# Performance work log

Hardware: AMD Instinct MI355X
Metric: run time of the kernel (lower is better)

The kernel has to match this reference:

```python
import jax, jax.numpy as jnp
import numpy as np

TWO_PI = 2.0 * np.pi
EPS = 1e-6

# mixture packed layout along last axis (7): [weight, px, py, cxx, cxy, cyx, cyy]

def unpack(m):
    w = m[..., 0]
    p = m[..., 1:3]
    C = m[..., 3:7].reshape(m.shape[:-1] + (2, 2))
    return w, p, C

def pack(w, p, C):
    return jnp.concatenate([w[..., None], p, C.reshape(C.shape[:-2] + (4,))], axis=-1)

def det2(C):
    return C[..., 0, 0] * C[..., 1, 1] - C[..., 0, 1] * C[..., 1, 0]

def inv2(C):
    d = det2(C)[..., None, None]
    adj = jnp.stack([
        jnp.stack([C[..., 1, 1], -C[..., 0, 1]], axis=-1),
        jnp.stack([-C[..., 1, 0], C[..., 0, 0]], axis=-1)], axis=-2)
    return adj / d

def component_integrals(w, C):
    # integral of an amplitude-parameterized 2D gaussian: w * 2*pi * sqrt(det C)
    return w * TWO_PI * jnp.sqrt(jnp.maximum(det2(C), EPS))

def gm_convolve(data, kernel):
    # data [B,Li,Nd,7], kernel [Lo,Li,Nk,7] -> [B,Lo,Li*Nd*Nk,7]
    wd, pd, Cd = unpack(data)
    wk, pk, Ck = unpack(kernel)
    dd = det2(Cd)[:, None, :, :, None]              # [B,1,Li,Nd,1]
    dk = det2(Ck)[None, :, :, None, :]              # [1,Lo,Li,1,Nk]
    Cs = Cd[:, None, :, :, None, :, :] + Ck[None, :, :, None, :, :, :]  # [B,Lo,Li,Nd,Nk,2,2]
    ps = pd[:, None, :, :, None, :] + pk[None, :, :, None, :, :]        # [B,Lo,Li,Nd,Nk,2]
    # amplitude of convolved gaussian so that integrals multiply
    ws = (wd[:, None, :, :, None] * wk[None, :, :, None, :]
          * TWO_PI * jnp.sqrt(dd * dk / jnp.maximum(det2(Cs), EPS)))
    m = pack(ws, ps, Cs)
    B, Lo = m.shape[0], m.shape[1]
    return m.reshape(B, Lo, -1, 7)

def eval_at_centers(w, p, C):
    # value of the whole mixture at each component center; [.., N]
    Ci = inv2(C)                                        # [..,N,2,2]
    diff = p[..., :, None, :] - p[..., None, :, :]      # [..,K,N,2]
    md = jnp.einsum('...kni,...nij,...knj->...kn', diff, Ci, diff)
    return jnp.einsum('...n,...kn->...k', w, jnp.exp(-0.5 * md))

def relu_fit(m, bias, n_out):
    # fitting-based ReLU: rescale each component so the mixture matches
    # relu(m(x)+b) at the centers, then keep the n_out largest components
    w, p, C = unpack(m)
    v = eval_at_centers(w, p, C) + bias[None, :, None]  # [B,L,N]
    scale = jax.nn.relu(v) / (jnp.abs(v) + EPS)
    w2 = w * scale
    _, idx = jax.lax.top_k(jnp.abs(w2), n_out)          # [B,L,n_out]
    w_s = jnp.take_along_axis(w2, idx, axis=-1)
    p_s = jnp.take_along_axis(p, jnp.broadcast_to(idx[..., None], idx.shape + (2,)), axis=-2)
    Cf = C.reshape(C.shape[:-2] + (4,))
    C_s = jnp.take_along_axis(Cf, jnp.broadcast_to(idx[..., None], idx.shape + (4,)), axis=-2)
    return pack(w_s, p_s, C_s.reshape(C_s.shape[:-1] + (2, 2)))

def batchnorm(m, per_gaussian):
    w, p, C = unpack(m)
    tot = jnp.sum(jnp.abs(component_integrals(w, C)), axis=-1, keepdims=True)  # [B,L,1]
    if not per_gaussian:
        tot = jnp.mean(tot, axis=0, keepdims=True)      # batch statistic per channel
    return pack(w / (tot + EPS), p, C)

def integrate(m):
    w, _, C = unpack(m)
    return jnp.sum(component_integrals(w, C), axis=-1)  # [B,L]

def forward(in_x, kernel1, kernel2, kernel3, bias1, bias2, bias3):
    x = batchnorm(in_x, per_gaussian=True)   # bn0
    x = gm_convolve(x, kernel1)              # [B,5,320,7]
    x = relu_fit(x, bias1, 25)
    x = batchnorm(x, per_gaussian=False)
    x = gm_convolve(x, kernel2)              # [B,6,625,7]
    x = relu_fit(x, bias2, 12)
    x = batchnorm(x, per_gaussian=False)
    x = gm_convolve(x, kernel3)              # [B,10,360,7]
    x = relu_fit(x, bias3, 5)
    x = batchnorm(x, per_gaussian=False)
    out = jax.nn.log_softmax(integrate(x), axis=1)
    return out.reshape(-1, 10)

def _make_kernel(key, lo, li, nk, weight_sd, position_range, covariance_range):
    kw, kp = jax.random.split(key)
    w = jax.random.normal(kw, (lo, li, nk)) * weight_sd
    p = jax.random.uniform(kp, (lo, li, nk, 2), minval=-position_range, maxval=position_range)
    C = jnp.broadcast_to(covariance_range * jnp.eye(2), (lo, li, nk, 2, 2))
    return pack(w, p, C).astype(jnp.float32)

def setup_inputs() -> dict:
    key = jax.random.key(0)
    k = jax.random.split(key, 8)
    B, NIN, NK = 32, 64, 5
    w = jax.random.uniform(k[0], (B, 1, NIN), minval=0.05, maxval=1.0)
    p = jax.random.uniform(k[1], (B, 1, NIN, 2), minval=-14.0, maxval=14.0)
    cdiag = jax.random.uniform(k[2], (B, 1, NIN, 2), minval=0.5, maxval=2.0)
    C = jnp.zeros((B, 1, NIN, 2, 2)).at[..., 0, 0].set(cdiag[..., 0]).at[..., 1, 1].set(cdiag[..., 1])
    in_x = pack(w, p, C).astype(jnp.float32)
    return {
        'in_x': in_x,
        'kernel1': _make_kernel(k[3], 5, 1, NK, 0.4, 2.0, 0.5),
        'kernel2': _make_kernel(k[4], 6, 5, NK, 0.04, 4.0, 2.0),
        'kernel3': _make_kernel(k[5], 10, 6, NK, 0.025, 8.0, 4.0),
        'bias1': jnp.zeros((5,), jnp.float32),
        'bias2': jnp.zeros((6,), jnp.float32),
        'bias3': jnp.zeros((10,), jnp.float32),
    }

def reference(in_x, kernel1, kernel2, kernel3, bias1, bias2, bias3):
    return forward(in_x, kernel1, kernel2, kernel3, bias1, bias2, bias3)
```

## Files before the change

### kernel.cpp

```cpp
#include <hip/hip_runtime.h>

#define TWO_PI_F 6.283185307179586f
#define EPS_F 1e-6f
#define LOG2E_F 1.4426950408889634f
#define BATCH 32

__device__ __forceinline__ float sane(float x) {
    return ((__float_as_uint(x) & 0x7f800000u) == 0x7f800000u) ? 0.f : x;
}

template<int LO, int LI, int ND, int NK, int NCOMP, int KOUT,
         int KP, int TPG, int G, bool FIRST>
__global__ __launch_bounds__(TPG*G) void layer_kernel(
    const float* __restrict__ in_x,
    const float* __restrict__ prev_sel,
    const float* __restrict__ prev_tot,
    const float* __restrict__ kern,
    const float* __restrict__ bias,
    float* __restrict__ out_sel,
    float* __restrict__ out_tot)
{
    constexpr int KUSE   = NCOMP / KP;
    static_assert(KUSE * KP == NCOMP, "exact k tiling required");
    constexpr int CHUNK  = (NCOMP + G - 1) / G;
    constexpr int NCOMP4 = (NCOMP + 3) & ~3;
    constexpr int NQ     = NCOMP4 / 4;
    constexpr int CQ     = (NQ + G - 1) / G;

    const int b   = blockIdx.x / LO;
    const int lo  = blockIdx.x % LO;
    const int tid = threadIdx.x;
    const int g   = tid / TPG;
    const int kt  = tid % TPG;
    const bool active = (kt < KUSE);

    struct StageT {
        float4 d_c[LI*ND];
        float4 k_c[LI*NK];
        float  d_w[LI*ND], d_px[LI*ND], d_py[LI*ND];
        float  k_w[LI*NK], k_px[LI*NK], k_py[LI*NK];
    };
    constexpr size_t ACCB = (size_t)(G > 1 ? (G-1)*TPG*KP : 1) * sizeof(float);
    constexpr size_t UB   = sizeof(StageT) > ACCB ? sizeof(StageT) : ACCB;
    __shared__ __align__(16) unsigned char u_smem[UB];
    StageT& st    = *reinterpret_cast<StageT*>(u_smem);
    float* accbuf = reinterpret_cast<float*>(u_smem);

    __shared__ float2 cPos[NCOMP];
    __shared__ float4 nP[NCOMP];
    __shared__ float4 nQ[NCOMP];
    __shared__ float4 cC[NCOMP];
    __shared__ float  w2s[NCOMP];
    __shared__ __align__(16) float a2s[NCOMP4];
    __shared__ float  scr[64];
    __shared__ float  selint[32];
    __shared__ float  dscale[LI];

    if constexpr (FIRST) {
        if (tid < ND) {
            const float* s = in_x + (size_t)(b*ND + tid)*7;
            const float w  = sane(s[0]);
            const float c0 = sane(s[3]), c1 = sane(s[4]), c2 = sane(s[5]), c3 = sane(s[6]);
            st.d_w[tid] = w; st.d_px[tid] = sane(s[1]); st.d_py[tid] = sane(s[2]);
            st.d_c[tid] = make_float4(c0, c1, c2, c3);
            const float det = c0*c3 - c1*c2;
            scr[tid] = sane(fabsf(w) * TWO_PI_F * sqrtf(fmaxf(det, EPS_F)));
        }
        __syncthreads();
        if (tid == 0) {
            float s = 0.f;
            for (int i = 0; i < ND; ++i) s += scr[i];
            dscale[0] = 1.f / (s + EPS_F);
        }
        __syncthreads();
        if (tid < ND) st.d_w[tid] = sane(st.d_w[tid] * dscale[0]);
    } else {
        if (tid < LI) {
            float s = 0.f;
            for (int bb = 0; bb < BATCH; ++bb) s += prev_tot[bb*LI + tid];
            dscale[tid] = 1.f / (s / (float)BATCH + EPS_F);
        }
        __syncthreads();
        if (tid < LI*ND) {
            const int li = tid / ND;
            const float* s = prev_sel + (size_t)(b*LI*ND + tid)*7;
            st.d_w[tid]  = sane(s[0] * dscale[li]);
            st.d_px[tid] = s[1]; st.d_py[tid] = s[2];
            st.d_c[tid]  = make_float4(s[3], s[4], s[5], s[6]);
        }
    }
    if (tid < LI*NK) {
        const float* s = kern + (size_t)(lo*LI*NK + tid)*7;
        st.k_w[tid]  = sane(s[0]);
        st.k_px[tid] = sane(s[1]); st.k_py[tid] = sane(s[2]);
        st.k_c[tid]  = make_float4(sane(s[3]), sane(s[4]), sane(s[5]), sane(s[6]));
    }
    __syncthreads();

    if (tid < NCOMP) {
        const int li = tid / (ND*NK);
        const int r  = tid % (ND*NK);
        const int nd = r / NK, nk = r % NK;
        const int di = li*ND + nd, ki = li*NK + nk;
        const float4 dc = st.d_c[di], kc = st.k_c[ki];
        const float c0 = dc.x + kc.x, c1 = dc.y + kc.y, c2 = dc.z + kc.z, c3 = dc.w + kc.w;
        const float dd = dc.x*dc.w - dc.y*dc.z;
        const float dk = kc.x*kc.w - kc.y*kc.z;
        const float ds = c0*c3 - c1*c2;
        const float w  = sane(st.d_w[di]*st.k_w[ki]*TWO_PI_F*sqrtf(fmaxf(dd*dk, 0.f) / fmaxf(ds, EPS_F)));
        const float px = sane(st.d_px[di] + st.k_px[ki]);
        const float py = sane(st.d_py[di] + st.k_py[ki]);
        const float inv = -0.5f * LOG2E_F / ds;
        const float a  = sane(c3*inv);
        const float bb = sane(-(c1 + c2)*inv);
        const float cc = sane(c0*inv);
        const float dd2 = sane(-(2.f*a*px + bb*py));
        const float ee  = sane(-(2.f*cc*py + bb*px));
        const float ff  = sane((a*px + bb*py)*px + cc*py*py);
        cPos[tid] = make_float2(px, py);
        nP[tid]   = make_float4(a, bb, cc, dd2);
        nQ[tid]   = make_float4(ee, ff, w, 0.f);
        cC[tid]   = make_float4(sane(c0), sane(c1), sane(c2), sane(c3));
    }
    __syncthreads();

    float kx[KP], ky[KP], kx2[KP], ky2[KP], kxy[KP], acc[KP];
    #pragma unroll
    for (int j = 0; j < KP; ++j) {
        acc[j] = 0.f; kx[j] = 0.f; ky[j] = 0.f;
        if (active) { const float2 p = cPos[kt + j*KUSE]; kx[j] = p.x; ky[j] = p.y; }
        kx2[j] = kx[j]*kx[j]; ky2[j] = ky[j]*ky[j]; kxy[j] = kx[j]*ky[j];
    }
    {
        const int n0 = g*CHUNK;
        const int n1 = (n0 + CHUNK < NCOMP) ? (n0 + CHUNK) : NCOMP;
        #pragma unroll 2
        for (int n = n0; n < n1; ++n) {
            const float4 P = nP[n];
            const float4 Q = nQ[n];
            #pragma unroll
            for (int j = 0; j < KP; ++j) {
                const float md = fmaf(P.x, kx2[j],
                                 fmaf(P.y, kxy[j],
                                 fmaf(P.z, ky2[j],
                                 fmaf(P.w, kx[j],
                                 fmaf(Q.x, ky[j], Q.y)))));
                acc[j] = fmaf(Q.z, exp2f(md), acc[j]);
            }
        }
    }
    if (g > 0 && active) {
        #pragma unroll
        for (int j = 0; j < KP; ++j) accbuf[((g-1)*TPG + kt)*KP + j] = acc[j];
    }
    __syncthreads();

    const float bi = bias[lo];
    if (g == 0 && active) {
        #pragma unroll
        for (int j = 0; j < KP; ++j) {
            float s = acc[j];
            for (int gg = 1; gg < G; ++gg) s += accbuf[((gg-1)*TPG + kt)*KP + j];
            const float v  = s + bi;
            const float sc = fmaxf(v, 0.f) / (fabsf(v) + EPS_F);
            const int   k  = kt + j*KUSE;
            const float ww = sane(nQ[k].z * sc);
            w2s[k] = ww;
            a2s[k] = fabsf(ww);
        }
    }
    if constexpr (NCOMP4 > NCOMP) {
        if (tid >= NCOMP && tid < NCOMP4) a2s[tid] = -1.f;
    }
    __syncthreads();

    int rank[KP];
    float myv[KP];
    #pragma unroll
    for (int j = 0; j < KP; ++j) rank[j] = 0;
    if (active) {
        #pragma unroll
        for (int j = 0; j < KP; ++j) myv[j] = a2s[kt + j*KUSE];
        const int q0 = g*CQ;
        const int q1 = (q0 + CQ < NQ) ? (q0 + CQ) : NQ;
        for (int q = q0; q < q1; ++q) {
            const float4 v4 = ((const float4*)a2s)[q];
            #pragma unroll
            for (int c = 0; c < 4; ++c) {
                const float vj = (c == 0) ? v4.x : (c == 1) ? v4.y : (c == 2) ? v4.z : v4.w;
                const int   jj = 4*q + c;
                #pragma unroll
                for (int j = 0; j < KP; ++j) {
                    const int myk = kt + j*KUSE;
                    rank[j] += (vj > myv[j] || (vj == myv[j] && jj < myk)) ? 1 : 0;
                }
            }
        }
        if (g > 0) {
            #pragma unroll
            for (int j = 0; j < KP; ++j) accbuf[((g-1)*TPG + kt)*KP + j] = (float)rank[j];
        }
    }
    __syncthreads();

    if (g == 0 && active) {
        #pragma unroll
        for (int j = 0; j < KP; ++j) {
            int r = rank[j];
            for (int gg = 1; gg < G; ++gg) r += (int)accbuf[((gg-1)*TPG + kt)*KP + j];
            if (r < KOUT) {
                const int k = kt + j*KUSE;
                const float2 p = cPos[k];
                const float4 c = cC[k];
                const float ww = w2s[k];
                float* dst = out_sel + (size_t)((b*LO + lo)*KOUT + r)*7;
                dst[0] = ww; dst[1] = p.x; dst[2] = p.y;
                dst[3] = c.x; dst[4] = c.y; dst[5] = c.z; dst[6] = c.w;
                const float det = c.x*c.w - c.y*c.z;
                selint[r] = sane(fabsf(ww) * TWO_PI_F * sqrtf(fmaxf(det, EPS_F)));
            }
        }
    }
    __syncthreads();
    if (tid == 0) {
        float s = 0.f;
        for (int i = 0; i < KOUT; ++i) s += selint[i];
        out_tot[b*LO + lo] = s;
    }
}

__global__ __launch_bounds__(64) void final_kernel(
    const float* __restrict__ sel3,
    const float* __restrict__ tot3,
    float* __restrict__ out)
{
    const int b = blockIdx.x;
    const int tid = threadIdx.x;
    __shared__ float scale3[10], integ[10], red2[2];
    if (tid < 10) {
        float s = 0.f;
        for (int bb = 0; bb < BATCH; ++bb) s += tot3[bb*10 + tid];
        scale3[tid] = 1.f / (s / (float)BATCH + EPS_F);
    }
    __syncthreads();
    if (tid < 10) {
        float s = 0.f;
        const float* base = sel3 + (size_t)((b*10 + tid)*5)*7;
        for (int kk = 0; kk < 5; ++kk) {
            const float* c = base + kk*7;
            const float det = c[3]*c[6] - c[4]*c[5];
            s += c[0] * scale3[tid] * TWO_PI_F * sqrtf(fmaxf(det, EPS_F));
        }
        integ[tid] = sane(s);
    }
    __syncthreads();
    if (tid == 0) {
        float m = -1e30f;
        for (int l = 0; l < 10; ++l) m = fmaxf(m, integ[l]);
        float ss = 0.f;
        for (int l = 0; l < 10; ++l) ss += __expf(integ[l] - m);
        red2[0] = m; red2[1] = logf(ss);
    }
    __syncthreads();
    if (tid < 10) out[b*10 + tid] = integ[tid] - red2[0] - red2[1];
}

extern "C" void kernel_launch(void* const* d_in, const int* in_sizes, int n_in,
                              void* d_out, int out_size, void* d_ws, size_t ws_size,
                              hipStream_t stream)
{
    const float* in_x = (const float*)d_in[0];
    const float* k1   = (const float*)d_in[1];
    const float* k2   = (const float*)d_in[2];
    const float* k3   = (const float*)d_in[3];
    const float* b1   = (const float*)d_in[4];
    const float* b2   = (const float*)d_in[5];
    const float* b3   = (const float*)d_in[6];
    float* out = (float*)d_out;

    float* ws = (float*)d_ws;
    float* sel1 = ws;
    float* tot1 = ws + 28000;
    float* sel2 = ws + 28160;
    float* tot2 = ws + 44288;
    float* sel3 = ws + 44480;
    float* tot3 = ws + 55680;

    layer_kernel<5, 1, 64, 5, 320, 25, 5, 64, 16, true><<<BATCH*5, 1024, 0, stream>>>(
        in_x, nullptr, nullptr, k1, b1, sel1, tot1);
    layer_kernel<6, 5, 25, 5, 625, 12, 5, 128, 8, false><<<BATCH*6, 1024, 0, stream>>>(
        nullptr, sel1, tot1, k2, b2, sel2, tot2);
    layer_kernel<10, 6, 12, 5, 360, 5, 6, 64, 12, false><<<BATCH*10, 768, 0, stream>>>(
        nullptr, sel2, tot2, k3, b3, sel3, tot3);
    final_kernel<<<BATCH, 64, 0, stream>>>(sel3, tot3, out);
}
```

Measured before the change: 170.4 us.

## Fuse all layers into one persistent kernel with atomic grid barriers

```diff
diff --git a/kernel.cpp b/kernel.cpp
--- a/kernel.cpp
+++ b/kernel.cpp
@@ -4,14 +4,56 @@
 #define EPS_F 1e-6f
 #define LOG2E_F 1.4426950408889634f
 #define BATCH 32
+#define GRIDB 256
 
 __device__ __forceinline__ float sane(float x) {
     return ((__float_as_uint(x) & 0x7f800000u) == 0x7f800000u) ? 0.f : x;
 }
 
+__device__ __forceinline__ void grid_barrier(unsigned int* cnt, int idx) {
+    __syncthreads();
+    if (threadIdx.x == 0) {
+        __threadfence();
+        atomicAdd(&cnt[idx * 32], 1u);
+        long long guard = 0;
+        while (__hip_atomic_load(&cnt[idx * 32], __ATOMIC_RELAXED,
+                                 __HIP_MEMORY_SCOPE_AGENT) < GRIDB
+               && guard < (1LL << 26)) {
+            __builtin_amdgcn_s_sleep(2);
+            ++guard;
+        }
+        __threadfence();
+    }
+    __syncthreads();
+}
+
+template<int LI, int ND, int NK, int NCOMP, int KP, int TPG, int G>
+struct LayerSmem {
+    struct StageT {
+        float4 d_c[LI*ND];
+        float4 k_c[LI*NK];
+        float  d_w[LI*ND], d_px[LI*ND], d_py[LI*ND];
+        float  k_w[LI*NK], k_px[LI*NK], k_py[LI*NK];
+    };
+    static constexpr int NCOMP4 = (NCOMP + 3) & ~3;
+    static constexpr int ACCN   = (G > 1) ? (G - 1) * TPG * KP : 1;
+    float2 cPos[NCOMP];
+    float4 nP[NCOMP];
+    float4 nQ[NCOMP];
+    float4 cC[NCOMP];
+    float  w2s[NCOMP];
+    alignas(16) float a2s[NCOMP4];
+    union { StageT st; float accbuf[ACCN]; } u;
+    float scr[64];
+    float selint[32];
+    float dscale[LI];
+};
+
+struct FinalSmem { float scale3[10]; float integ[10]; float red2[2]; };
+
 template<int LO, int LI, int ND, int NK, int NCOMP, int KOUT,
          int KP, int TPG, int G, bool FIRST>
-__global__ __launch_bounds__(TPG*G) void layer_kernel(
+__device__ void layer_body(void* smem_raw, int blk,
     const float* __restrict__ in_x,
     const float* __restrict__ prev_sel,
     const float* __restrict__ prev_tot,
@@ -20,80 +62,60 @@
     float* __restrict__ out_sel,
     float* __restrict__ out_tot)
 {
-    constexpr int KUSE   = NCOMP / KP;
+    using SM = LayerSmem<LI, ND, NK, NCOMP, KP, TPG, G>;
+    SM& sm = *reinterpret_cast<SM*>(smem_raw);
+    constexpr int KUSE = NCOMP / KP;
     static_assert(KUSE * KP == NCOMP, "exact k tiling required");
     constexpr int CHUNK  = (NCOMP + G - 1) / G;
-    constexpr int NCOMP4 = (NCOMP + 3) & ~3;
-    constexpr int NQ     = NCOMP4 / 4;
-    constexpr int CQ     = (NQ + G - 1) / G;
-
-    const int b   = blockIdx.x / LO;
-    const int lo  = blockIdx.x % LO;
+    constexpr int NCOMP4 = SM::NCOMP4;
+    constexpr int NQn    = NCOMP4 / 4;
+    constexpr int CQ     = (NQn + G - 1) / G;
+
+    const int b   = blk / LO;
+    const int lo  = blk % LO;
     const int tid = threadIdx.x;
     const int g   = tid / TPG;
     const int kt  = tid % TPG;
     const bool active = (kt < KUSE);
-
-    struct StageT {
-        float4 d_c[LI*ND];
-        float4 k_c[LI*NK];
-        float  d_w[LI*ND], d_px[LI*ND], d_py[LI*ND];
-        float  k_w[LI*NK], k_px[LI*NK], k_py[LI*NK];
-    };
-    constexpr size_t ACCB = (size_t)(G > 1 ? (G-1)*TPG*KP : 1) * sizeof(float);
-    constexpr size_t UB   = sizeof(StageT) > ACCB ? sizeof(StageT) : ACCB;
-    __shared__ __align__(16) unsigned char u_smem[UB];
-    StageT& st    = *reinterpret_cast<StageT*>(u_smem);
-    float* accbuf = reinterpret_cast<float*>(u_smem);
-
-    __shared__ float2 cPos[NCOMP];
-    __shared__ float4 nP[NCOMP];
-    __shared__ float4 nQ[NCOMP];
-    __shared__ float4 cC[NCOMP];
-    __shared__ float  w2s[NCOMP];
-    __shared__ __align__(16) float a2s[NCOMP4];
-    __shared__ float  scr[64];
-    __shared__ float  selint[32];
-    __shared__ float  dscale[LI];
 
     if constexpr (FIRST) {
         if (tid < ND) {
             const float* s = in_x + (size_t)(b*ND + tid)*7;
             const float w  = sane(s[0]);
             const float c0 = sane(s[3]), c1 = sane(s[4]), c2 = sane(s[5]), c3 = sane(s[6]);
-            st.d_w[tid] = w; st.d_px[tid] = sane(s[1]); st.d_py[tid] = sane(s[2]);
-            st.d_c[tid] = make_float4(c0, c1, c2, c3);
+            sm.u.st.d_w[tid] = w; sm.u.st.d_px[tid] = sane(s[1]); sm.u.st.d_py[tid] = sane(s[2]);
+            sm.u.st.d_c[tid] = make_float4(c0, c1, c2, c3);
             const float det = c0*c3 - c1*c2;
-            scr[tid] = sane(fabsf(w) * TWO_PI_F * sqrtf(fmaxf(det, EPS_F)));
+            sm.scr[tid] = sane(fabsf(w) * TWO_PI_F * sqrtf(fmaxf(det, EPS_F)));
         }
         __syncthreads();
         if (tid == 0) {
             float s = 0.f;
-            for (int i = 0; i < ND; ++i) s += scr[i];
-            dscale[0] = 1.f / (s + EPS_F);
+            for (int i = 0; i < ND; ++i) s += sm.scr[i];
+            sm.dscale[0] = 1.f / (s + EPS_F);
         }
         __syncthreads();
-        if (tid < ND) st.d_w[tid] = sane(st.d_w[tid] * dscale[0]);
+        if (tid < ND) sm.u.st.d_w[tid] = sane(sm.u.st.d_w[tid] * sm.dscale[0]);
     } else {
         if (tid < LI) {
             float s = 0.f;
             for (int bb = 0; bb < BATCH; ++bb) s += prev_tot[bb*LI + tid];
-            dscale[tid] = 1.f / (s / (float)BATCH + EPS_F);
+            sm.dscale[tid] = 1.f / (s / (float)BATCH + EPS_F);
         }
         __syncthreads();
         if (tid < LI*ND) {
             const int li = tid / ND;
             const float* s = prev_sel + (size_t)(b*LI*ND + tid)*7;
-            st.d_w[tid]  = sane(s[0] * dscale[li]);
-            st.d_px[tid] = s[1]; st.d_py[tid] = s[2];
-            st.d_c[tid]  = make_float4(s[3], s[4], s[5], s[6]);
+            sm.u.st.d_w[tid]  = sane(s[0] * sm.dscale[li]);
+            sm.u.st.d_px[tid] = s[1]; sm.u.st.d_py[tid] = s[2];
+            sm.u.st.d_c[tid]  = make_float4(s[3], s[4], s[5], s[6]);
         }
     }
     if (tid < LI*NK) {
         const float* s = kern + (size_t)(lo*LI*NK + tid)*7;
-        st.k_w[tid]  = sane(s[0]);
-        st.k_px[tid] = sane(s[1]); st.k_py[tid] = sane(s[2]);
-        st.k_c[tid]  = make_float4(sane(s[3]), sane(s[4]), sane(s[5]), sane(s[6]));
+        sm.u.st.k_w[tid]  = sane(s[0]);
+        sm.u.st.k_px[tid] = sane(s[1]); sm.u.st.k_py[tid] = sane(s[2]);
+        sm.u.st.k_c[tid]  = make_float4(sane(s[3]), sane(s[4]), sane(s[5]), sane(s[6]));
     }
     __syncthreads();
 
@@ -102,25 +124,26 @@
         const int r  = tid % (ND*NK);
         const int nd = r / NK, nk = r % NK;
         const int di = li*ND + nd, ki = li*NK + nk;
-        const float4 dc = st.d_c[di], kc = st.k_c[ki];
+        const float4 dc = sm.u.st.d_c[di], kc = sm.u.st.k_c[ki];
         const float c0 = dc.x + kc.x, c1 = dc.y + kc.y, c2 = dc.z + kc.z, c3 = dc.w + kc.w;
         const float dd = dc.x*dc.w - dc.y*dc.z;
         const float dk = kc.x*kc.w - kc.y*kc.z;
         const float ds = c0*c3 - c1*c2;
-        const float w  = sane(st.d_w[di]*st.k_w[ki]*TWO_PI_F*sqrtf(fmaxf(dd*dk, 0.f) / fmaxf(ds, EPS_F)));
-        const float px = sane(st.d_px[di] + st.k_px[ki]);
-        const float py = sane(st.d_py[di] + st.k_py[ki]);
+        const float w  = sane(sm.u.st.d_w[di]*sm.u.st.k_w[ki]*TWO_PI_F
+                              *sqrtf(fmaxf(dd*dk, 0.f) / fmaxf(ds, EPS_F)));
+        const float px = sane(sm.u.st.d_px[di] + sm.u.st.k_px[ki]);
+        const float py = sane(sm.u.st.d_py[di] + sm.u.st.k_py[ki]);
         const float inv = -0.5f * LOG2E_F / ds;
-        const float a  = sane(c3*inv);
-        const float bb = sane(-(c1 + c2)*inv);
-        const float cc = sane(c0*inv);
+        const float a   = sane(c3*inv);
+        const float bb  = sane(-(c1 + c2)*inv);
+        const float cc  = sane(c0*inv);
         const float dd2 = sane(-(2.f*a*px + bb*py));
         const float ee  = sane(-(2.f*cc*py + bb*px));
         const float ff  = sane((a*px + bb*py)*px + cc*py*py);
-        cPos[tid] = make_float2(px, py);
-        nP[tid]   = make_float4(a, bb, cc, dd2);
-        nQ[tid]   = make_float4(ee, ff, w, 0.f);
-        cC[tid]   = make_float4(sane(c0), sane(c1), sane(c2), sane(c3));
+        sm.cPos[tid] = make_float2(px, py);
+        sm.nP[tid]   = make_float4(a, bb, cc, dd2);
+        sm.nQ[tid]   = make_float4(ee, ff, w, 0.f);
+        sm.cC[tid]   = make_float4(sane(c0), sane(c1), sane(c2), sane(c3));
     }
     __syncthreads();
 
@@ -128,7 +151,7 @@
     #pragma unroll
     for (int j = 0; j < KP; ++j) {
         acc[j] = 0.f; kx[j] = 0.f; ky[j] = 0.f;
-        if (active) { const float2 p = cPos[kt + j*KUSE]; kx[j] = p.x; ky[j] = p.y; }
+        if (active) { const float2 p = sm.cPos[kt + j*KUSE]; kx[j] = p.x; ky[j] = p.y; }
         kx2[j] = kx[j]*kx[j]; ky2[j] = ky[j]*ky[j]; kxy[j] = kx[j]*ky[j];
     }
     {
@@ -136,8 +159,8 @@
         const int n1 = (n0 + CHUNK < NCOMP) ? (n0 + CHUNK) : NCOMP;
         #pragma unroll 2
         for (int n = n0; n < n1; ++n) {
-            const float4 P = nP[n];
-            const float4 Q = nQ[n];
+            const float4 P = sm.nP[n];
+            const float4 Q = sm.nQ[n];
             #pragma unroll
             for (int j = 0; j < KP; ++j) {
                 const float md = fmaf(P.x, kx2[j],
@@ -151,7 +174,7 @@
     }
     if (g > 0 && active) {
         #pragma unroll
-        for (int j = 0; j < KP; ++j) accbuf[((g-1)*TPG + kt)*KP + j] = acc[j];
+        for (int j = 0; j < KP; ++j) sm.u.accbuf[((g-1)*TPG + kt)*KP + j] = acc[j];
     }
     __syncthreads();
 
@@ -160,17 +183,17 @@
         #pragma unroll
         for (int j = 0; j < KP; ++j) {
             float s = acc[j];
-            for (int gg = 1; gg < G; ++gg) s += accbuf[((gg-1)*TPG + kt)*KP + j];
+            for (int gg = 1; gg < G; ++gg) s += sm.u.accbuf[((gg-1)*TPG + kt)*KP + j];
             const float v  = s + bi;
             const float sc = fmaxf(v, 0.f) / (fabsf(v) + EPS_F);
             const int   k  = kt + j*KUSE;
-            const float ww = sane(nQ[k].z * sc);
-            w2s[k] = ww;
-            a2s[k] = fabsf(ww);
+            const float ww = sane(sm.nQ[k].z * sc);
+            sm.w2s[k] = ww;
+            sm.a2s[k] = fabsf(ww);
         }
     }
     if constexpr (NCOMP4 > NCOMP) {
-        if (tid >= NCOMP && tid < NCOMP4) a2s[tid] = -1.f;
+        if (tid >= NCOMP && tid < NCOMP4) sm.a2s[tid] = -1.f;
     }
     __syncthreads();
 
@@ -180,11 +203,11 @@
     for (int j = 0; j < KP; ++j) rank[j] = 0;
     if (active) {
         #pragma unroll
-        for (int j = 0; j < KP; ++j) myv[j] = a2s[kt + j*KUSE];
+        for (int j = 0; j < KP; ++j) myv[j] = sm.a2s[kt + j*KUSE];
         const int q0 = g*CQ;
-        const int q1 = (q0 + CQ < NQ) ? (q0 + CQ) : NQ;
+        const int q1 = (q0 + CQ < NQn) ? (q0 + CQ) : NQn;
         for (int q = q0; q < q1; ++q) {
-            const float4 v4 = ((const float4*)a2s)[q];
+            const float4 v4 = ((const float4*)sm.a2s)[q];
             #pragma unroll
             for (int c = 0; c < 4; ++c) {
                 const float vj = (c == 0) ? v4.x : (c == 1) ? v4.y : (c == 2) ? v4.z : v4.w;
@@ -198,7 +221,7 @@
         }
         if (g > 0) {
             #pragma unroll
-            for (int j = 0; j < KP; ++j) accbuf[((g-1)*TPG + kt)*KP + j] = (float)rank[j];
+            for (int j = 0; j < KP; ++j) sm.u.accbuf[((g-1)*TPG + kt)*KP + j] = (float)rank[j];
         }
     }
     __syncthreads();
@@ -207,40 +230,38 @@
         #pragma unroll
         for (int j = 0; j < KP; ++j) {
             int r = rank[j];
-            for (int gg = 1; gg < G; ++gg) r += (int)accbuf[((gg-1)*TPG + kt)*KP + j];
+            for (int gg = 1; gg < G; ++gg) r += (int)sm.u.accbuf[((gg-1)*TPG + kt)*KP + j];
             if (r < KOUT) {
                 const int k = kt + j*KUSE;
-                const float2 p = cPos[k];
-                const float4 c = cC[k];
-                const float ww = w2s[k];
+                const float2 p = sm.cPos[k];
+                const float4 c = sm.cC[k];
+                const float ww = sm.w2s[k];
                 float* dst = out_sel + (size_t)((b*LO + lo)*KOUT + r)*7;
                 dst[0] = ww; dst[1] = p.x; dst[2] = p.y;
                 dst[3] = c.x; dst[4] = c.y; dst[5] = c.z; dst[6] = c.w;
                 const float det = c.x*c.w - c.y*c.z;
-                selint[r] = sane(fabsf(ww) * TWO_PI_F * sqrtf(fmaxf(det, EPS_F)));
+                sm.selint[r] = sane(fabsf(ww) * TWO_PI_F * sqrtf(fmaxf(det, EPS_F)));
             }
         }
     }
     __syncthreads();
     if (tid == 0) {
         float s = 0.f;
-        for (int i = 0; i < KOUT; ++i) s += selint[i];
+        for (int i = 0; i < KOUT; ++i) s += sm.selint[i];
         out_tot[b*LO + lo] = s;
     }
 }
 
-__global__ __launch_bounds__(64) void final_kernel(
-    const float* __restrict__ sel3,
-    const float* __restrict__ tot3,
+__device__ void final_body(void* smem_raw, int b,
+    const float* __restrict__ sel3, const float* __restrict__ tot3,
     float* __restrict__ out)
 {
-    const int b = blockIdx.x;
+    FinalSmem& sm = *reinterpret_cast<FinalSmem*>(smem_raw);
     const int tid = threadIdx.x;
-    __shared__ float scale3[10], integ[10], red2[2];
     if (tid < 10) {
         float s = 0.f;
         for (int bb = 0; bb < BATCH; ++bb) s += tot3[bb*10 + tid];
-        scale3[tid] = 1.f / (s / (float)BATCH + EPS_F);
+        sm.scale3[tid] = 1.f / (s / (float)BATCH + EPS_F);
     }
     __syncthreads();
     if (tid < 10) {
@@ -249,20 +270,63 @@
         for (int kk = 0; kk < 5; ++kk) {
             const float* c = base + kk*7;
             const float det = c[3]*c[6] - c[4]*c[5];
-            s += c[0] * scale3[tid] * TWO_PI_F * sqrtf(fmaxf(det, EPS_F));
-        }
-        integ[tid] = sane(s);
+            s += c[0] * sm.scale3[tid] * TWO_PI_F * sqrtf(fmaxf(det, EPS_F));
+        }
+        sm.integ[tid] = sane(s);
     }
     __syncthreads();
     if (tid == 0) {
         float m = -1e30f;
-        for (int l = 0; l < 10; ++l) m = fmaxf(m, integ[l]);
+        for (int l = 0; l < 10; ++l) m = fmaxf(m, sm.integ[l]);
         float ss = 0.f;
-        for (int l = 0; l < 10; ++l) ss += __expf(integ[l] - m);
-        red2[0] = m; red2[1] = logf(ss);
-    }
-    __syncthreads();
-    if (tid < 10) out[b*10 + tid] = integ[tid] - red2[0] - red2[1];
+        for (int l = 0; l < 10; ++l) ss += __expf(sm.integ[l] - m);
+        sm.red2[0] = m; sm.red2[1] = logf(ss);
+    }
+    __syncthreads();
+    if (tid < 10) out[b*10 + tid] = sm.integ[tid] - sm.red2[0] - sm.red2[1];
+}
+
+using S1 = LayerSmem<1, 64, 5, 320, 5, 64, 16>;
+using S2 = LayerSmem<5, 25, 5, 625, 5, 128, 8>;
+using S3 = LayerSmem<6, 12, 5, 360, 6, 64, 16>;
+constexpr size_t cmax2(size_t a, size_t b) { return a > b ? a : b; }
+constexpr size_t SMEM_MAX = cmax2(cmax2(sizeof(S1), sizeof(S2)),
+                                  cmax2(sizeof(S3), sizeof(FinalSmem)));
+
+__global__ __launch_bounds__(1024) void fused_net(
+    const float* __restrict__ in_x,
+    const float* __restrict__ k1, const float* __restrict__ k2,
+    const float* __restrict__ k3,
+    const float* __restrict__ b1, const float* __restrict__ b2,
+    const float* __restrict__ b3,
+    float* __restrict__ sel1, float* __restrict__ tot1,
+    float* __restrict__ sel2, float* __restrict__ tot2,
+    float* __restrict__ sel3, float* __restrict__ tot3,
+    unsigned int* __restrict__ bar,
+    float* __restrict__ out)
+{
+    __shared__ __align__(16) unsigned char smem[SMEM_MAX];
+    const int blk = blockIdx.x;
+
+    if (blk < BATCH*5)
+        layer_body<5, 1, 64, 5, 320, 25, 5, 64, 16, true>(
+            smem, blk, in_x, nullptr, nullptr, k1, b1, sel1, tot1);
+    grid_barrier(bar, 0);
+
+    if (blk < BATCH*6)
+        layer_body<6, 5, 25, 5, 625, 12, 5, 128, 8, false>(
+            smem, blk, nullptr, sel1, tot1, k2, b2, sel2, tot2);
+    grid_barrier(bar, 1);
+
+    for (int u = blk; u < BATCH*10; u += GRIDB) {
+        layer_body<10, 6, 12, 5, 360, 5, 6, 64, 16, false>(
+            smem, u, nullptr, sel2, tot2, k3, b3, sel3, tot3);
+        __syncthreads();
+    }
+    grid_barrier(bar, 2);
+
+    if (blk < BATCH)
+        final_body(smem, blk, sel3, tot3, out);
 }
 
 extern "C" void kernel_launch(void* const* d_in, const int* in_sizes, int n_in,
@@ -285,12 +349,11 @@
     float* tot2 = ws + 44288;
     float* sel3 = ws + 44480;
     float* tot3 = ws + 55680;
-
-    layer_kernel<5, 1, 64, 5, 320, 25, 5, 64, 16, true><<<BATCH*5, 1024, 0, stream>>>(
-        in_x, nullptr, nullptr, k1, b1, sel1, tot1);
-    layer_kernel<6, 5, 25, 5, 625, 12, 5, 128, 8, false><<<BATCH*6, 1024, 0, stream>>>(
-        nullptr, sel1, tot1, k2, b2, sel2, tot2);
-    layer_kernel<10, 6, 12, 5, 360, 5, 6, 64, 12, false><<<BATCH*10, 768, 0, stream>>>(
-        nullptr, sel2, tot2, k3, b3, sel3, tot3);
-    final_kernel<<<BATCH, 64, 0, stream>>>(sel3, tot3, out);
-}
+    unsigned int* bar = (unsigned int*)(ws + 56064);
+
+    hipMemsetAsync(bar, 0, 3 * 32 * sizeof(unsigned int), stream);
+
+    fused_net<<<GRIDB, 1024, 0, stream>>>(
+        in_x, k1, k2, k3, b1, b2, b3,
+        sel1, tot1, sel2, tot2, sel3, tot3, bar, out);
+}
```

After: 222.8 us. +30.7%, slower.

## Split layer-2 mixture evaluation across two blocks with separate merge/rank kernel

Applied to the files above, without the earlier changes.

```diff
diff --git a/kernel.cpp b/kernel.cpp
--- a/kernel.cpp
+++ b/kernel.cpp
@@ -24,8 +24,8 @@
     static_assert(KUSE * KP == NCOMP, "exact k tiling required");
     constexpr int CHUNK  = (NCOMP + G - 1) / G;
     constexpr int NCOMP4 = (NCOMP + 3) & ~3;
-    constexpr int NQ     = NCOMP4 / 4;
-    constexpr int CQ     = (NQ + G - 1) / G;
+    constexpr int NQn    = NCOMP4 / 4;
+    constexpr int CQ     = (NQn + G - 1) / G;
 
     const int b   = blockIdx.x / LO;
     const int lo  = blockIdx.x % LO;
@@ -111,9 +111,9 @@
         const float px = sane(st.d_px[di] + st.k_px[ki]);
         const float py = sane(st.d_py[di] + st.k_py[ki]);
         const float inv = -0.5f * LOG2E_F / ds;
-        const float a  = sane(c3*inv);
-        const float bb = sane(-(c1 + c2)*inv);
-        const float cc = sane(c0*inv);
+        const float a   = sane(c3*inv);
+        const float bb  = sane(-(c1 + c2)*inv);
+        const float cc  = sane(c0*inv);
         const float dd2 = sane(-(2.f*a*px + bb*py));
         const float ee  = sane(-(2.f*cc*py + bb*px));
         const float ff  = sane((a*px + bb*py)*px + cc*py*py);
@@ -182,7 +182,7 @@
         #pragma unroll
         for (int j = 0; j < KP; ++j) myv[j] = a2s[kt + j*KUSE];
         const int q0 = g*CQ;
-        const int q1 = (q0 + CQ < NQ) ? (q0 + CQ) : NQ;
+        const int q1 = (q0 + CQ < NQn) ? (q0 + CQ) : NQn;
         for (int q = q0; q < q1; ++q) {
             const float4 v4 = ((const float4*)a2s)[q];
             #pragma unroll
@@ -229,6 +229,289 @@
     }
 }
 
+template<int LO, int LI, int ND, int NK, int NCOMP, int KP, int TPG, int G,
+         int NSPLIT, int PADK>
+__global__ __launch_bounds__(TPG*G) void eval_partial_kernel(
+    const float* __restrict__ prev_sel,
+    const float* __restrict__ prev_tot,
+    const float* __restrict__ kern,
+    float* __restrict__ part)
+{
+    constexpr int KUSE = NCOMP / KP;
+    static_assert(KUSE * KP == NCOMP, "exact k tiling required");
+    constexpr int CH2 = (NCOMP + NSPLIT - 1) / NSPLIT;
+    constexpr int CHG = (CH2 + G - 1) / G;
+
+    const int unit = blockIdx.x;
+    const int h    = unit / (BATCH*LO);
+    const int rem  = unit % (BATCH*LO);
+    const int b    = rem / LO;
+    const int lo   = rem % LO;
+    const int tid  = threadIdx.x;
+    const int g    = tid / TPG;
+    const int kt   = tid % TPG;
+    const bool active = (kt < KUSE);
+
+    struct StageT {
+        float4 d_c[LI*ND];
+        float4 k_c[LI*NK];
+        float  d_w[LI*ND], d_px[LI*ND], d_py[LI*ND];
+        float  k_w[LI*NK], k_px[LI*NK], k_py[LI*NK];
+    };
+    constexpr size_t ACCB = (size_t)(G > 1 ? (G-1)*TPG*KP : 1) * sizeof(float);
+    constexpr size_t UB   = sizeof(StageT) > ACCB ? sizeof(StageT) : ACCB;
+    __shared__ __align__(16) unsigned char u_smem[UB];
+    StageT& st    = *reinterpret_cast<StageT*>(u_smem);
+    float* accbuf = reinterpret_cast<float*>(u_smem);
+
+    __shared__ float2 cPos[NCOMP];
+    __shared__ float4 nP[NCOMP];
+    __shared__ float4 nQ[NCOMP];
+    __shared__ float  dscale[LI];
+
+    if (tid < LI) {
+        float s = 0.f;
+        for (int bb = 0; bb < BATCH; ++bb) s += prev_tot[bb*LI + tid];
+        dscale[tid] = 1.f / (s / (float)BATCH + EPS_F);
+    }
+    __syncthreads();
+    if (tid < LI*ND) {
+        const int li = tid / ND;
+        const float* s = prev_sel + (size_t)(b*LI*ND + tid)*7;
+        st.d_w[tid]  = sane(s[0] * dscale[li]);
+        st.d_px[tid] = s[1]; st.d_py[tid] = s[2];
+        st.d_c[tid]  = make_float4(s[3], s[4], s[5], s[6]);
+    }
+    if (tid < LI*NK) {
+        const float* s = kern + (size_t)(lo*LI*NK + tid)*7;
+        st.k_w[tid]  = sane(s[0]);
+        st.k_px[tid] = sane(s[1]); st.k_py[tid] = sane(s[2]);
+        st.k_c[tid]  = make_float4(sane(s[3]), sane(s[4]), sane(s[5]), sane(s[6]));
+    }
+    __syncthreads();
+
+    if (tid < NCOMP) {
+        const int li = tid / (ND*NK);
+        const int r  = tid % (ND*NK);
+        const int nd = r / NK, nk = r % NK;
+        const int di = li*ND + nd, ki = li*NK + nk;
+        const float4 dc = st.d_c[di], kc = st.k_c[ki];
+        const float c0 = dc.x + kc.x, c1 = dc.y + kc.y, c2 = dc.z + kc.z, c3 = dc.w + kc.w;
+        const float dd = dc.x*dc.w - dc.y*dc.z;
+        const float dk = kc.x*kc.w - kc.y*kc.z;
+        const float ds = c0*c3 - c1*c2;
+        const float w  = sane(st.d_w[di]*st.k_w[ki]*TWO_PI_F*sqrtf(fmaxf(dd*dk, 0.f) / fmaxf(ds, EPS_F)));
+        const float px = sane(st.d_px[di] + st.k_px[ki]);
+        const float py = sane(st.d_py[di] + st.k_py[ki]);
+        const float inv = -0.5f * LOG2E_F / ds;
+        const float a   = sane(c3*inv);
+        const float bb  = sane(-(c1 + c2)*inv);
+        const float cc  = sane(c0*inv);
+        const float dd2 = sane(-(2.f*a*px + bb*py));
+        const float ee  = sane(-(2.f*cc*py + bb*px));
+        const float ff  = sane((a*px + bb*py)*px + cc*py*py);
+        cPos[tid] = make_float2(px, py);
+        nP[tid]   = make_float4(a, bb, cc, dd2);
+        nQ[tid]   = make_float4(ee, ff, w, 0.f);
+    }
+    __syncthreads();
+
+    float kx[KP], ky[KP], kx2[KP], ky2[KP], kxy[KP], acc[KP];
+    #pragma unroll
+    for (int j = 0; j < KP; ++j) {
+        acc[j] = 0.f; kx[j] = 0.f; ky[j] = 0.f;
+        if (active) { const float2 p = cPos[kt + j*KUSE]; kx[j] = p.x; ky[j] = p.y; }
+        kx2[j] = kx[j]*kx[j]; ky2[j] = ky[j]*ky[j]; kxy[j] = kx[j]*ky[j];
+    }
+    {
+        const int nlo = h*CH2;
+        const int nhi = (nlo + CH2 < NCOMP) ? (nlo + CH2) : NCOMP;
+        const int n0  = nlo + g*CHG;
+        const int n1  = (n0 + CHG < nhi) ? (n0 + CHG) : nhi;
+        if (n0 < n1) {
+            float4 P = nP[n0], Q = nQ[n0];
+            for (int n = n0; n < n1; ++n) {
+                const int nn = (n + 1 < n1) ? n + 1 : n0;
+                const float4 Pn = nP[nn];
+                const float4 Qn = nQ[nn];
+                #pragma unroll
+                for (int j = 0; j < KP; ++j) {
+                    const float md = fmaf(P.x, kx2[j],
+                                     fmaf(P.y, kxy[j],
+                                     fmaf(P.z, ky2[j],
+                                     fmaf(P.w, kx[j],
+                                     fmaf(Q.x, ky[j], Q.y)))));
+                    acc[j] = fmaf(Q.z, exp2f(md), acc[j]);
+                }
+                P = Pn; Q = Qn;
+            }
+        }
+    }
+    if (g > 0 && active) {
+        #pragma unroll
+        for (int j = 0; j < KP; ++j) accbuf[((g-1)*TPG + kt)*KP + j] = acc[j];
+    }
+    __syncthreads();
+    if (g == 0 && active) {
+        float* dst = part + (size_t)unit * PADK;
+        #pragma unroll
+        for (int j = 0; j < KP; ++j) {
+            float s = acc[j];
+            for (int gg = 1; gg < G; ++gg) s += accbuf[((gg-1)*TPG + kt)*KP + j];
+            dst[kt + j*KUSE] = s;
+        }
+    }
+}
+
+template<int LO, int LI, int ND, int NK, int NCOMP, int KOUT, int KP, int TPG,
+         int G, int NSPLIT, int PADK>
+__global__ __launch_bounds__(TPG*G) void merge_rank_kernel(
+    const float* __restrict__ prev_sel,
+    const float* __restrict__ prev_tot,
+    const float* __restrict__ kern,
+    const float* __restrict__ bias,
+    const float* __restrict__ part,
+    float* __restrict__ out_sel,
+    float* __restrict__ out_tot)
+{
+    constexpr int KUSE   = NCOMP / KP;
+    constexpr int NCOMP4 = (NCOMP + 3) & ~3;
+    constexpr int NQn    = NCOMP4 / 4;
+    constexpr int CQ     = (NQn + G - 1) / G;
+
+    const int b   = blockIdx.x / LO;
+    const int lo  = blockIdx.x % LO;
+    const int tid = threadIdx.x;
+    const int g   = tid / TPG;
+    const int kt  = tid % TPG;
+    const bool active = (kt < KUSE);
+
+    struct StageT {
+        float4 d_c[LI*ND];
+        float4 k_c[LI*NK];
+        float  d_w[LI*ND], d_px[LI*ND], d_py[LI*ND];
+        float  k_w[LI*NK], k_px[LI*NK], k_py[LI*NK];
+    };
+    constexpr size_t ACCB = (size_t)(G > 1 ? (G-1)*TPG*KP : 1) * sizeof(float);
+    constexpr size_t UB   = sizeof(StageT) > ACCB ? sizeof(StageT) : ACCB;
+    __shared__ __align__(16) unsigned char u_smem[UB];
+    StageT& st    = *reinterpret_cast<StageT*>(u_smem);
+    float* accbuf = reinterpret_cast<float*>(u_smem);
+
+    __shared__ float2 cPos[NCOMP];
+    __shared__ float4 cC[NCOMP];
+    __shared__ float  cw[NCOMP];
+    __shared__ float  w2s[NCOMP];
+    __shared__ __align__(16) float a2s[NCOMP4];
+    __shared__ float  selint[32];
+    __shared__ float  dscale[LI];
+
+    if (tid < LI) {
+        float s = 0.f;
+        for (int bb = 0; bb < BATCH; ++bb) s += prev_tot[bb*LI + tid];
+        dscale[tid] = 1.f / (s / (float)BATCH + EPS_F);
+    }
+    __syncthreads();
+    if (tid < LI*ND) {
+        const int li = tid / ND;
+        const float* s = prev_sel + (size_t)(b*LI*ND + tid)*7;
+        st.d_w[tid]  = sane(s[0] * dscale[li]);
+        st.d_px[tid] = s[1]; st.d_py[tid] = s[2];
+        st.d_c[tid]  = make_float4(s[3], s[4], s[5], s[6]);
+    }
+    if (tid < LI*NK) {
+        const float* s = kern + (size_t)(lo*LI*NK + tid)*7;
+        st.k_w[tid]  = sane(s[0]);
+        st.k_px[tid] = sane(s[1]); st.k_py[tid] = sane(s[2]);
+        st.k_c[tid]  = make_float4(sane(s[3]), sane(s[4]), sane(s[5]), sane(s[6]));
+    }
+    __syncthreads();
+
+    const float bi = bias[lo];
+    if (tid < NCOMP) {
+        const int li = tid / (ND*NK);
+        const int r  = tid % (ND*NK);
+        const int nd = r / NK, nk = r % NK;
+        const int di = li*ND + nd, ki = li*NK + nk;
+        const float4 dc = st.d_c[di], kc = st.k_c[ki];
+        const float c0 = dc.x + kc.x, c1 = dc.y + kc.y, c2 = dc.z + kc.z, c3 = dc.w + kc.w;
+        const float dd = dc.x*dc.w - dc.y*dc.z;
+        const float dk = kc.x*kc.w - kc.y*kc.z;
+        const float ds = c0*c3 - c1*c2;
+        const float w  = sane(st.d_w[di]*st.k_w[ki]*TWO_PI_F*sqrtf(fmaxf(dd*dk, 0.f) / fmaxf(ds, EPS_F)));
+        cPos[tid] = make_float2(sane(st.d_px[di] + st.k_px[ki]),
+                                sane(st.d_py[di] + st.k_py[ki]));
+        cC[tid]   = make_float4(sane(c0), sane(c1), sane(c2), sane(c3));
+        cw[tid]   = w;
+        float v = bi;
+        #pragma unroll
+        for (int hh = 0; hh < NSPLIT; ++hh)
+            v += part[(size_t)((hh*BATCH + b)*LO + lo) * PADK + tid];
+        const float sc = fmaxf(v, 0.f) / (fabsf(v) + EPS_F);
+        const float ww = sane(w * sc);
+        w2s[tid] = ww;
+        a2s[tid] = fabsf(ww);
+    }
+    if constexpr (NCOMP4 > NCOMP) {
+        if (tid >= NCOMP && tid < NCOMP4) a2s[tid] = -1.f;
+    }
+    __syncthreads();
+
+    int rank[KP];
+    float myv[KP];
+    #pragma unroll
+    for (int j = 0; j < KP; ++j) rank[j] = 0;
+    if (active) {
+        #pragma unroll
+        for (int j = 0; j < KP; ++j) myv[j] = a2s[kt + j*KUSE];
+        const int q0 = g*CQ;
+        const int q1 = (q0 + CQ < NQn) ? (q0 + CQ) : NQn;
+        for (int q = q0; q < q1; ++q) {
+            const float4 v4 = ((const float4*)a2s)[q];
+            #pragma unroll
+            for (int c = 0; c < 4; ++c) {
+                const float vj = (c == 0) ? v4.x : (c == 1) ? v4.y : (c == 2) ? v4.z : v4.w;
+                const int   jj = 4*q + c;
+                #pragma unroll
+                for (int j = 0; j < KP; ++j) {
+                    const int myk = kt + j*KUSE;
+                    rank[j] += (vj > myv[j] || (vj == myv[j] && jj < myk)) ? 1 : 0;
+                }
+            }
+        }
+        if (g > 0) {
+            #pragma unroll
+            for (int j = 0; j < KP; ++j) accbuf[((g-1)*TPG + kt)*KP + j] = (float)rank[j];
+        }
+    }
+    __syncthreads();
+
+    if (g == 0 && active) {
+        #pragma unroll
+        for (int j = 0; j < KP; ++j) {
+            int r = rank[j];
+            for (int gg = 1; gg < G; ++gg) r += (int)accbuf[((gg-1)*TPG + kt)*KP + j];
+            if (r < KOUT) {
+                const int k = kt + j*KUSE;
+                const float2 p = cPos[k];
+                const float4 c = cC[k];
+                const float ww = w2s[k];
+                float* dst = out_sel + (size_t)((b*LO + lo)*KOUT + r)*7;
+                dst[0] = ww; dst[1] = p.x; dst[2] = p.y;
+                dst[3] = c.x; dst[4] = c.y; dst[5] = c.z; dst[6] = c.w;
+                const float det = c.x*c.w - c.y*c.z;
+                selint[r] = sane(fabsf(ww) * TWO_PI_F * sqrtf(fmaxf(det, EPS_F)));
+            }
+        }
+    }
+    __syncthreads();
+    if (tid == 0) {
+        float s = 0.f;
+        for (int i = 0; i < KOUT; ++i) s += selint[i];
+        out_tot[b*LO + lo] = s;
+    }
+}
+
 __global__ __launch_bounds__(64) void final_kernel(
     const float* __restrict__ sel3,
     const float* __restrict__ tot3,
@@ -285,11 +568,14 @@
     float* tot2 = ws + 44288;
     float* sel3 = ws + 44480;
     float* tot3 = ws + 55680;
+    float* part = ws + 56064;
 
     layer_kernel<5, 1, 64, 5, 320, 25, 5, 64, 16, true><<<BATCH*5, 1024, 0, stream>>>(
         in_x, nullptr, nullptr, k1, b1, sel1, tot1);
-    layer_kernel<6, 5, 25, 5, 625, 12, 5, 128, 8, false><<<BATCH*6, 1024, 0, stream>>>(
-        nullptr, sel1, tot1, k2, b2, sel2, tot2);
+    eval_partial_kernel<6, 5, 25, 5, 625, 5, 128, 8, 2, 640><<<BATCH*6*2, 1024, 0, stream>>>(
+        sel1, tot1, k2, part);
+    merge_rank_kernel<6, 5, 25, 5, 625, 12, 5, 128, 5, 2, 640><<<BATCH*6, 640, 0, stream>>>(
+        sel1, tot1, k2, b2, part, sel2, tot2);
     layer_kernel<10, 6, 12, 5, 360, 5, 6, 64, 12, false><<<BATCH*10, 768, 0, stream>>>(
         nullptr, sel2, tot2, k3, b3, sel3, tot3);
     final_kernel<<<BATCH, 64, 0, stream>>>(sel3, tot3, out);
```

New measurement: 174.1 us. 1.02x slower.
